# Optimization experiments

Hardware: AMD Instinct MI355X
Metric: run time of the kernel (lower is better)

## Reference

```python
import jax, jax.numpy as jnp
import numpy as np

BATCH, SEQ, D_IN = 4, 2048, 1024
STATE, D_OUT, KX = 1024, 1024, 10


def setup_inputs() -> dict:
    key = jax.random.key(0)
    k0, k1, k2, k3, k4, k5 = jax.random.split(key, 6)
    inputs = jax.random.normal(k0, (BATCH, SEQ, D_IN), jnp.float32)
    h0 = jax.random.normal(k1, (STATE,), jnp.float32)
    A = jax.random.normal(k2, (STATE,), jnp.float32)
    A = A / jnp.max(jnp.abs(A))  # matches init_A / max|init_A|
    B = jax.random.normal(k3, (D_IN, STATE), jnp.float32) / D_IN
    C = jax.random.normal(k4, (STATE, D_OUT), jnp.float32) / STATE
    M = jax.random.normal(k5, (D_IN, D_OUT, KX), jnp.float32) / D_OUT
    return {"inputs": inputs, "h0": h0, "A": A, "B": B, "C": C, "M": M}


def compute_ar_x_preds(w, x):
    # w: (d_out, d_in, k); x: (b, l, d_in)
    d_out, d_in, k = w.shape
    b, l, _ = x.shape
    o = jnp.einsum('oik,bli->bklo', w, x)  # (b, k, l, d_out)
    shifts = jnp.arange(k)
    # roll slice i forward by i along the length axis
    o = jax.vmap(lambda oi, s: jnp.roll(oi, s, axis=1), in_axes=(1, 0), out_axes=1)(o, shifts)
    # triu mask: keep position t in slice i only if t >= i (causal AR)
    m = (jnp.arange(l)[None, :] >= shifts[:, None]).astype(o.dtype)  # (k, l)
    return jnp.sum(o * m[None, :, :, None], axis=1)  # (b, l, d_out)


def reference(inputs, h0, A, B, C, M):
    bsz = inputs.shape[0]
    h_init = jnp.broadcast_to(h0, (bsz, h0.shape[0]))  # h0.expand(bsz, state_dim)
    u_seq = jnp.swapaxes(inputs, 0, 1)  # (l, b, d_in)

    def step(h, u):
        h_new = A * h + u @ B  # diagonal recurrence
        return h_new, h_new

    _, hs = jax.lax.scan(step, h_init, u_seq)  # (l, b, state)
    all_h_t = jnp.swapaxes(hs, 0, 1)  # (b, l, state)
    lds_out = all_h_t @ C  # (b, l, d_out)
    ar = compute_ar_x_preds(M, inputs)
    return lds_out + ar
```

## Files before the change

kernel.cpp:

```cpp
#include <hip/hip_runtime.h>
#include <stdint.h>

typedef unsigned short u16;
typedef __attribute__((ext_vector_type(4))) float f32x4;
typedef __attribute__((ext_vector_type(8))) short s16x8;

#define BATCH 4
#define SEQ   2048
#define DIM   1024
#define KX    10
#define PAD   16
#define SEQP  (SEQ+PAD)

__device__ __forceinline__ u16 f2b(float f) {
    union { float f; uint32_t u; } v; v.f = f;
    uint32_t u = v.u + 0x7fffu + ((v.u >> 16) & 1u);
    return (u16)(u >> 16);
}
__device__ __forceinline__ float b2f(u16 h) {
    union { uint32_t u; float f; } v; v.u = ((uint32_t)h) << 16;
    return v.f;
}

__device__ __forceinline__ void llds16(const u16* g, u16* l) {
    __builtin_amdgcn_global_load_lds(
        (const __attribute__((address_space(1))) uint32_t*)g,
        (__attribute__((address_space(3))) uint32_t*)l, 16, 0, 0);
}

#define PREP_X_END  8256
#define PREP_C_END  10304
#define PREP_M_END  14400

__global__ __launch_bounds__(256) void k_prep(
    const float* __restrict__ x, const float* __restrict__ B,
    const float* __restrict__ C, const float* __restrict__ M,
    u16* __restrict__ Xpad, u16* __restrict__ Btr, u16* __restrict__ Wall)
{
    __shared__ float tile[32][33];
    const int bid = blockIdx.x, tid = threadIdx.x;

    if (bid < PREP_X_END) {
        int idx = bid * 256 + tid;
        long e = (long)idx * 4;
        int i = (int)(e & 1023);
        int row = (int)(e >> 10);
        int t = row % SEQP;
        int b = row / SEQP;
        ushort4 o;
        if (t < PAD) {
            o.x = 0; o.y = 0; o.z = 0; o.w = 0;
        } else {
            const float4 v = *(const float4*)(x + (((long)(b * SEQ + (t - PAD)) << 10) + i));
            o.x = f2b(v.x); o.y = f2b(v.y); o.z = f2b(v.z); o.w = f2b(v.w);
        }
        *(ushort4*)(Xpad + ((long)row << 10) + i) = o;
    } else if (bid < PREP_C_END) {
        const int tb = bid - PREP_X_END;
        const float* in = (tb < 1024) ? B : C;
        u16* out = (tb < 1024) ? Btr : Wall;
        int lb = tb & 1023;
        int bx = lb & 31, by = lb >> 5;
        int tx = tid & 31, ty = tid >> 5;
#pragma unroll
        for (int j = 0; j < 4; j++)
            tile[ty + j * 8][tx] = in[(long)(by * 32 + ty + j * 8) * 1024 + bx * 32 + tx];
        __syncthreads();
#pragma unroll
        for (int j = 0; j < 4; j++)
            out[(long)(bx * 32 + ty + j * 8) * 1024 + by * 32 + tx] = f2b(tile[tx][ty + j * 8]);
    } else {
        int idx = (bid - PREP_C_END) * 256 + tid;
        int o = idx >> 10, i = idx & 1023;
        const float* src = M + (long)idx * KX;
#pragma unroll
        for (int k = 0; k < KX; k++)
            Wall[((long)(k + 1) << 20) + ((long)o << 10) + i] = f2b(src[k]);
    }
}


__global__ void k_scan1(const u16* __restrict__ U, const float* __restrict__ A,
                        float* __restrict__ F) {
    const int sg = threadIdx.x;
    const int bc = blockIdx.x;
    const int b = bc >> 5, c = bc & 31;
    const int s0 = sg << 3;
    const float4 a0 = *(const float4*)(A + s0);
    const float4 a1 = *(const float4*)(A + s0 + 4);
    float a[8] = {a0.x, a0.y, a0.z, a0.w, a1.x, a1.y, a1.z, a1.w};
    float f[8] = {0.f, 0.f, 0.f, 0.f, 0.f, 0.f, 0.f, 0.f};
    const u16* u = U + (((long)(b * SEQ + c * 64)) << 10) + s0;
#pragma unroll 4
    for (int j = 0; j < 64; j++) {
        s16x8 v = *(const s16x8*)(u + ((long)j << 10));
#pragma unroll
        for (int i = 0; i < 8; i++) f[i] = fmaf(a[i], f[i], b2f((u16)v[i]));
    }
    *(float4*)(F + ((long)bc << 10) + s0)     = (float4){f[0], f[1], f[2], f[3]};
    *(float4*)(F + ((long)bc << 10) + s0 + 4) = (float4){f[4], f[5], f[6], f[7]};
}

__global__ void k_scan2(const float* __restrict__ F, const float* __restrict__ A,
                        const float* __restrict__ h0, float* __restrict__ Carry) {
    int idx = blockIdx.x * 256 + threadIdx.x;
    int b = idx >> 10, s = idx & 1023;
    float a = A[s];
    float a64 = a;
#pragma unroll
    for (int q = 0; q < 6; q++) a64 *= a64;
    float carry = h0[s];
#pragma unroll
    for (int c = 0; c < 32; c++) {
        long off = ((long)(b * 32 + c) << 10) + s;
        Carry[off] = carry;
        carry = fmaf(a64, carry, F[off]);
    }
}

__global__ void k_scan3(u16* __restrict__ U, const float* __restrict__ A,
                        const float* __restrict__ Carry) {
    const int sg = threadIdx.x;
    const int bc = blockIdx.x;
    const int b = bc >> 5, c = bc & 31;
    const int s0 = sg << 3;
    const float4 a0 = *(const float4*)(A + s0);
    const float4 a1 = *(const float4*)(A + s0 + 4);
    float a[8] = {a0.x, a0.y, a0.z, a0.w, a1.x, a1.y, a1.z, a1.w};
    float h[8];
#pragma unroll
    for (int i = 0; i < 8; i++) h[i] = Carry[((long)bc << 10) + s0 + i];
    u16* u = U + (((long)(b * SEQ + c * 64)) << 10) + s0;
#pragma unroll 4
    for (int j = 0; j < 64; j++) {
        s16x8 v = *(const s16x8*)(u + ((long)j << 10));
        s16x8 w;
#pragma unroll
        for (int i = 0; i < 8; i++) {
            h[i] = fmaf(a[i], h[i], b2f((u16)v[i]));
            w[i] = (short)f2b(h[i]);
        }
        *(s16x8*)(u + ((long)j << 10)) = w;
    }
}

__global__ __launch_bounds__(256, 4) void k_gemm(
    void* __restrict__ outv, const u16* __restrict__ Xpad,
    const u16* __restrict__ Hbf, const u16* __restrict__ W,
    int ngroups, int use_h, int bf16_out)
{
    __shared__ u16 smem[18432];

    const int tid  = threadIdx.x;
    const int wave = tid >> 6, lane = tid & 63;
    const int pair = wave >> 1, wm = wave & 1;
    const int quad = lane >> 4, l15 = lane & 15;

    const int col0 = blockIdx.x * 64;
    const int row0 = blockIdx.y * 128;
    const int bb = row0 >> 11;
    const long Xrow0 = (long)bb * SEQP + PAD + (row0 & (SEQ - 1));
    const long XslabBase = (Xrow0 - 16) << 10;
    const int lastg = ngroups - 1;

    f32x4 acc[4][4];
#pragma unroll
    for (int i = 0; i < 4; i++)
#pragma unroll
        for (int j = 0; j < 4; j++)
            acc[i][j] = (f32x4){0.f, 0.f, 0.f, 0.f};

    auto stageX2 = [&](int k0) {
#pragma unroll
        for (int p = 0; p < 2; p++) {
            const int kb = k0 + p * 512;
            u16* slab = smem + p * 5120;
#pragma unroll
            for (int q = 0; q < 2; q++) {
                int u = q * 256 + tid;
                int row = u >> 2;
                int kc = (u & 3) ^ ((row >> 1) & 3);
                llds16(Xpad + XslabBase + ((long)row << 10) + kb + kc * 8,
                       &slab[(q * 256 + wave * 64) * 8]);
            }
            {
                int u = 512 + tid;
                int row = u >> 2;
                int kc = (u & 3) ^ ((row >> 1) & 3);
                if (tid < 128)
                    llds16(Xpad + XslabBase + ((long)row << 10) + kb + kc * 8,
                           &slab[(512 + wave * 64) * 8]);
            }
        }
    };
    auto stageW2 = [&](int k0, int wsel, int parity) {
        const u16* Wg = W + ((long)wsel << 20) + ((long)col0 << 10);
#pragma unroll
        for (int p = 0; p < 2; p++) {
            int row = tid >> 2;
            int kc = (tid & 3) ^ ((row >> 1) & 3);
            llds16(Wg + ((long)row << 10) + (k0 + p * 512) + kc * 8,
                   &smem[10240 + (p * 2 + parity) * 2048 + wave * 64 * 8]);
        }
    };
    auto stageH2 = [&](int k0) {
        const u16* Hb = Hbf + ((long)row0 << 10);
#pragma unroll
        for (int p = 0; p < 2; p++) {
            const int kb = k0 + p * 512;
            u16* slab = smem + p * 5120;
#pragma unroll
            for (int q = 0; q < 2; q++) {
                int u = q * 256 + tid;
                int row = u >> 2;
                int kc = (u & 3) ^ ((row >> 1) & 3);
                llds16(Hb + ((long)row << 10) + kb + kc * 8,
                       &slab[(q * 256 + wave * 64) * 8]);
            }
        }
    };

    const u16* slab  = smem + pair * 5120;
    const u16* Wpair = smem + 10240 + pair * 2 * 2048;

    for (int k0 = 0; k0 < 512; k0 += 32) {
        stageX2(k0);
        stageW2(k0, use_h ? 1 : 0, 0);
        __syncthreads();

        for (int g = 0; g < ngroups; g++) {
            const bool isH = use_h && (g == lastg);
            if (isH) {
                stageH2(k0);
                __syncthreads();
            }
            if (g < lastg) {
                int gn = g + 1;
                int wsel = use_h ? ((gn == lastg) ? 0 : gn + 1) : gn;
                stageW2(k0, wsel, gn & 1);
            }

            const int rbase = isH ? 0 : (16 - g);
            const u16* Wrd = Wpair + (g & 1) * 2048;

            s16x8 af[4], bfr[4];
#pragma unroll
            for (int mi = 0; mi < 4; mi++) {
                int arow = rbase + wm * 64 + mi * 16 + l15;
                int kca = (quad ^ ((arow >> 1) & 3)) << 3;
                af[mi] = *(const s16x8*)&slab[arow * 32 + kca];
            }
#pragma unroll
            for (int ni = 0; ni < 4; ni++) {
                int brow = ni * 16 + l15;
                int kcb = (quad ^ ((brow >> 1) & 3)) << 3;
                bfr[ni] = *(const s16x8*)&Wrd[brow * 32 + kcb];
            }
#pragma unroll
            for (int mi = 0; mi < 4; mi++)
#pragma unroll
                for (int ni = 0; ni < 4; ni++)
                    acc[mi][ni] = __builtin_amdgcn_mfma_f32_16x16x32_bf16(
                        af[mi], bfr[ni], acc[mi][ni], 0, 0, 0);
            __syncthreads();
        }
    }

    float* scr = (float*)smem;
    if (pair == 1) {
#pragma unroll
        for (int mi = 0; mi < 4; mi++) {
            int rl = wm * 64 + mi * 16 + quad * 4;
#pragma unroll
            for (int ni = 0; ni < 4; ni++) {
                int c = ni * 16 + l15;
                f32x4 v = acc[mi][ni];
#pragma unroll
                for (int reg = 0; reg < 4; reg++)
                    scr[(rl + reg) * 64 + c] = v[reg];
            }
        }
    }
    __syncthreads();
    if (pair == 0) {
#pragma unroll
        for (int mi = 0; mi < 4; mi++) {
            int rl = wm * 64 + mi * 16 + quad * 4;
            int r = row0 + rl;
#pragma unroll
            for (int ni = 0; ni < 4; ni++) {
                int cl = ni * 16 + l15;
                int c = col0 + cl;
                f32x4 v = acc[mi][ni];
                if (bf16_out) {
                    u16* ob = (u16*)outv;
#pragma unroll
                    for (int reg = 0; reg < 4; reg++)
                        ob[((long)(r + reg) << 10) + c] =
                            f2b(v[reg] + scr[(rl + reg) * 64 + cl]);
                } else {
                    float* of = (float*)outv;
#pragma unroll
                    for (int reg = 0; reg < 4; reg++)
                        of[((long)(r + reg) << 10) + c] =
                            v[reg] + scr[(rl + reg) * 64 + cl];
                }
            }
        }
    }
}


extern "C" void kernel_launch(void* const* d_in, const int* in_sizes, int n_in,
                              void* d_out, int out_size, void* d_ws, size_t ws_size,
                              hipStream_t stream) {
    const float* x  = (const float*)d_in[0];
    const float* h0 = (const float*)d_in[1];
    const float* A  = (const float*)d_in[2];
    const float* B  = (const float*)d_in[3];
    const float* C  = (const float*)d_in[4];
    const float* M  = (const float*)d_in[5];
    float* out = (float*)d_out;

    char* ws = (char*)d_ws;
    u16*   Xpad  = (u16*)  (ws);
    u16*   Wall  = (u16*)  (ws + 16908288);
    u16*   Btr   = (u16*)  (ws + 39976960);
    u16*   Ubf   = (u16*)  (ws + 42074112);
    float* F     = (float*)(ws + 39976960);
    float* Carry = (float*)(ws + 39976960 + 524288);

    k_prep<<<dim3(PREP_M_END), dim3(256), 0, stream>>>(x, B, C, M, Xpad, Btr, Wall);

    k_gemm<<<dim3(16, 64), dim3(256), 0, stream>>>(Ubf, Xpad, Ubf, Btr, 1, 0, 1);

    k_scan1<<<dim3(128), dim3(128), 0, stream>>>(Ubf, A, F);
    k_scan2<<<dim3(16), dim3(256), 0, stream>>>(F, A, h0, Carry);
    k_scan3<<<dim3(128), dim3(128), 0, stream>>>(Ubf, A, Carry);

    k_gemm<<<dim3(16, 64), dim3(256), 0, stream>>>(out, Xpad, Ubf, Wall, 11, 1, 0);
}
```

Baseline: 354.6 us.

## Widen GEMM tile to 128 columns and split scan into finer chunks

The GEMM block tile grows from 128x64 to 128x128, so each wave holds 4x8 accumulators and reuses each A fragment across eight B fragments. This halves redundant X/H staging across column blocks at the cost of more registers, lower occupancy (launch bounds 2) and a two-pass epilogue with a padded scratch stride. Separately, the chunked scan uses 64 chunks of 32 steps instead of 32 of 64, doubling parallelism in the scan1/scan3 passes and lengthening the serial carry pass.

```diff
diff --git a/kernel.cpp b/kernel.cpp
--- a/kernel.cpp
+++ b/kernel.cpp
@@ -84,15 +84,15 @@
                         float* __restrict__ F) {
     const int sg = threadIdx.x;
     const int bc = blockIdx.x;
-    const int b = bc >> 5, c = bc & 31;
+    const int b = bc >> 6, c = bc & 63;
     const int s0 = sg << 3;
     const float4 a0 = *(const float4*)(A + s0);
     const float4 a1 = *(const float4*)(A + s0 + 4);
     float a[8] = {a0.x, a0.y, a0.z, a0.w, a1.x, a1.y, a1.z, a1.w};
     float f[8] = {0.f, 0.f, 0.f, 0.f, 0.f, 0.f, 0.f, 0.f};
-    const u16* u = U + (((long)(b * SEQ + c * 64)) << 10) + s0;
+    const u16* u = U + (((long)(b * SEQ + c * 32)) << 10) + s0;
 #pragma unroll 4
-    for (int j = 0; j < 64; j++) {
+    for (int j = 0; j < 32; j++) {
         s16x8 v = *(const s16x8*)(u + ((long)j << 10));
 #pragma unroll
         for (int i = 0; i < 8; i++) f[i] = fmaf(a[i], f[i], b2f((u16)v[i]));
@@ -106,15 +106,15 @@
     int idx = blockIdx.x * 256 + threadIdx.x;
     int b = idx >> 10, s = idx & 1023;
     float a = A[s];
-    float a64 = a;
-#pragma unroll
-    for (int q = 0; q < 6; q++) a64 *= a64;
+    float a32 = a;
+#pragma unroll
+    for (int q = 0; q < 5; q++) a32 *= a32;
     float carry = h0[s];
 #pragma unroll
-    for (int c = 0; c < 32; c++) {
-        long off = ((long)(b * 32 + c) << 10) + s;
+    for (int c = 0; c < 64; c++) {
+        long off = ((long)(b * 64 + c) << 10) + s;
         Carry[off] = carry;
-        carry = fmaf(a64, carry, F[off]);
+        carry = fmaf(a32, carry, F[off]);
     }
 }
 
@@ -122,7 +122,7 @@
                         const float* __restrict__ Carry) {
     const int sg = threadIdx.x;
     const int bc = blockIdx.x;
-    const int b = bc >> 5, c = bc & 31;
+    const int b = bc >> 6, c = bc & 63;
     const int s0 = sg << 3;
     const float4 a0 = *(const float4*)(A + s0);
     const float4 a1 = *(const float4*)(A + s0 + 4);
@@ -130,9 +130,9 @@
     float h[8];
 #pragma unroll
     for (int i = 0; i < 8; i++) h[i] = Carry[((long)bc << 10) + s0 + i];
-    u16* u = U + (((long)(b * SEQ + c * 64)) << 10) + s0;
+    u16* u = U + (((long)(b * SEQ + c * 32)) << 10) + s0;
 #pragma unroll 4
-    for (int j = 0; j < 64; j++) {
+    for (int j = 0; j < 32; j++) {
         s16x8 v = *(const s16x8*)(u + ((long)j << 10));
         s16x8 w;
 #pragma unroll
@@ -144,30 +144,30 @@
     }
 }
 
-__global__ __launch_bounds__(256, 4) void k_gemm(
+__global__ __launch_bounds__(256, 2) void k_gemm(
     void* __restrict__ outv, const u16* __restrict__ Xpad,
     const u16* __restrict__ Hbf, const u16* __restrict__ W,
     int ngroups, int use_h, int bf16_out)
 {
-    __shared__ u16 smem[18432];
+    __shared__ u16 smem[26624];
 
     const int tid  = threadIdx.x;
     const int wave = tid >> 6, lane = tid & 63;
     const int pair = wave >> 1, wm = wave & 1;
     const int quad = lane >> 4, l15 = lane & 15;
 
-    const int col0 = blockIdx.x * 64;
+    const int col0 = blockIdx.x * 128;
     const int row0 = blockIdx.y * 128;
     const int bb = row0 >> 11;
     const long Xrow0 = (long)bb * SEQP + PAD + (row0 & (SEQ - 1));
     const long XslabBase = (Xrow0 - 16) << 10;
     const int lastg = ngroups - 1;
 
-    f32x4 acc[4][4];
+    f32x4 acc[4][8];
 #pragma unroll
     for (int i = 0; i < 4; i++)
 #pragma unroll
-        for (int j = 0; j < 4; j++)
+        for (int j = 0; j < 8; j++)
             acc[i][j] = (f32x4){0.f, 0.f, 0.f, 0.f};
 
     auto stageX2 = [&](int k0) {
@@ -197,10 +197,14 @@
         const u16* Wg = W + ((long)wsel << 20) + ((long)col0 << 10);
 #pragma unroll
         for (int p = 0; p < 2; p++) {
-            int row = tid >> 2;
-            int kc = (tid & 3) ^ ((row >> 1) & 3);
-            llds16(Wg + ((long)row << 10) + (k0 + p * 512) + kc * 8,
-                   &smem[10240 + (p * 2 + parity) * 2048 + wave * 64 * 8]);
+#pragma unroll
+            for (int q = 0; q < 2; q++) {
+                int u = q * 256 + tid;
+                int row = u >> 2;
+                int kc = (u & 3) ^ ((row >> 1) & 3);
+                llds16(Wg + ((long)row << 10) + (k0 + p * 512) + kc * 8,
+                       &smem[10240 + (p * 2 + parity) * 4096 + (q * 256 + wave * 64) * 8]);
+            }
         }
     };
     auto stageH2 = [&](int k0) {
@@ -221,7 +225,7 @@
     };
 
     const u16* slab  = smem + pair * 5120;
-    const u16* Wpair = smem + 10240 + pair * 2 * 2048;
+    const u16* Wpair = smem + 10240 + pair * 2 * 4096;
 
     for (int k0 = 0; k0 < 512; k0 += 32) {
         stageX2(k0);
@@ -241,72 +245,76 @@
             }
 
             const int rbase = isH ? 0 : (16 - g);
-            const u16* Wrd = Wpair + (g & 1) * 2048;
-
-            s16x8 af[4], bfr[4];
+            const u16* Wrd = Wpair + (g & 1) * 4096;
+
+            s16x8 bfr[8];
+#pragma unroll
+            for (int ni = 0; ni < 8; ni++) {
+                int brow = ni * 16 + l15;
+                int kcb = (quad ^ ((brow >> 1) & 3)) << 3;
+                bfr[ni] = *(const s16x8*)&Wrd[brow * 32 + kcb];
+            }
 #pragma unroll
             for (int mi = 0; mi < 4; mi++) {
                 int arow = rbase + wm * 64 + mi * 16 + l15;
                 int kca = (quad ^ ((arow >> 1) & 3)) << 3;
-                af[mi] = *(const s16x8*)&slab[arow * 32 + kca];
-            }
-#pragma unroll
-            for (int ni = 0; ni < 4; ni++) {
-                int brow = ni * 16 + l15;
-                int kcb = (quad ^ ((brow >> 1) & 3)) << 3;
-                bfr[ni] = *(const s16x8*)&Wrd[brow * 32 + kcb];
-            }
-#pragma unroll
-            for (int mi = 0; mi < 4; mi++)
-#pragma unroll
-                for (int ni = 0; ni < 4; ni++)
+                s16x8 af = *(const s16x8*)&slab[arow * 32 + kca];
+#pragma unroll
+                for (int ni = 0; ni < 8; ni++)
                     acc[mi][ni] = __builtin_amdgcn_mfma_f32_16x16x32_bf16(
-                        af[mi], bfr[ni], acc[mi][ni], 0, 0, 0);
+                        af, bfr[ni], acc[mi][ni], 0, 0, 0);
+            }
             __syncthreads();
         }
     }
 
     float* scr = (float*)smem;
-    if (pair == 1) {
-#pragma unroll
-        for (int mi = 0; mi < 4; mi++) {
-            int rl = wm * 64 + mi * 16 + quad * 4;
-#pragma unroll
-            for (int ni = 0; ni < 4; ni++) {
-                int c = ni * 16 + l15;
-                f32x4 v = acc[mi][ni];
-#pragma unroll
-                for (int reg = 0; reg < 4; reg++)
-                    scr[(rl + reg) * 64 + c] = v[reg];
-            }
-        }
-    }
-    __syncthreads();
-    if (pair == 0) {
-#pragma unroll
-        for (int mi = 0; mi < 4; mi++) {
-            int rl = wm * 64 + mi * 16 + quad * 4;
-            int r = row0 + rl;
-#pragma unroll
-            for (int ni = 0; ni < 4; ni++) {
-                int cl = ni * 16 + l15;
-                int c = col0 + cl;
-                f32x4 v = acc[mi][ni];
-                if (bf16_out) {
-                    u16* ob = (u16*)outv;
+#pragma unroll
+    for (int half = 0; half < 2; half++) {
+        if (pair == 1) {
+#pragma unroll
+            for (int m2 = 0; m2 < 2; m2++) {
+                int mi = half * 2 + m2;
+                int rl = wm * 32 + m2 * 16 + quad * 4;
+#pragma unroll
+                for (int ni = 0; ni < 8; ni++) {
+                    int c = ni * 16 + l15;
+                    f32x4 v = acc[mi][ni];
 #pragma unroll
                     for (int reg = 0; reg < 4; reg++)
-                        ob[((long)(r + reg) << 10) + c] =
-                            f2b(v[reg] + scr[(rl + reg) * 64 + cl]);
-                } else {
-                    float* of = (float*)outv;
-#pragma unroll
-                    for (int reg = 0; reg < 4; reg++)
-                        of[((long)(r + reg) << 10) + c] =
-                            v[reg] + scr[(rl + reg) * 64 + cl];
+                        scr[(rl + reg) * 129 + c] = v[reg];
                 }
             }
         }
+        __syncthreads();
+        if (pair == 0) {
+#pragma unroll
+            for (int m2 = 0; m2 < 2; m2++) {
+                int mi = half * 2 + m2;
+                int rl = wm * 32 + m2 * 16 + quad * 4;
+                int r = row0 + wm * 64 + mi * 16 + quad * 4;
+#pragma unroll
+                for (int ni = 0; ni < 8; ni++) {
+                    int cl = ni * 16 + l15;
+                    int c = col0 + cl;
+                    f32x4 v = acc[mi][ni];
+                    if (bf16_out) {
+                        u16* ob = (u16*)outv;
+#pragma unroll
+                        for (int reg = 0; reg < 4; reg++)
+                            ob[((long)(r + reg) << 10) + c] =
+                                f2b(v[reg] + scr[(rl + reg) * 129 + cl]);
+                    } else {
+                        float* of = (float*)outv;
+#pragma unroll
+                        for (int reg = 0; reg < 4; reg++)
+                            of[((long)(r + reg) << 10) + c] =
+                                v[reg] + scr[(rl + reg) * 129 + cl];
+                    }
+                }
+            }
+        }
+        __syncthreads();
     }
 }
 
@@ -328,15 +336,15 @@
     u16*   Btr   = (u16*)  (ws + 39976960);
     u16*   Ubf   = (u16*)  (ws + 42074112);
     float* F     = (float*)(ws + 39976960);
-    float* Carry = (float*)(ws + 39976960 + 524288);
+    float* Carry = (float*)(ws + 39976960 + 1048576);
 
     k_prep<<<dim3(PREP_M_END), dim3(256), 0, stream>>>(x, B, C, M, Xpad, Btr, Wall);
 
-    k_gemm<<<dim3(16, 64), dim3(256), 0, stream>>>(Ubf, Xpad, Ubf, Btr, 1, 0, 1);
-
-    k_scan1<<<dim3(128), dim3(128), 0, stream>>>(Ubf, A, F);
+    k_gemm<<<dim3(8, 64), dim3(256), 0, stream>>>(Ubf, Xpad, Ubf, Btr, 1, 0, 1);
+
+    k_scan1<<<dim3(256), dim3(128), 0, stream>>>(Ubf, A, F);
     k_scan2<<<dim3(16), dim3(256), 0, stream>>>(F, A, h0, Carry);
-    k_scan3<<<dim3(128), dim3(128), 0, stream>>>(Ubf, A, Carry);
-
-    k_gemm<<<dim3(16, 64), dim3(256), 0, stream>>>(out, Xpad, Ubf, Wall, 11, 1, 0);
-}
+    k_scan3<<<dim3(256), dim3(128), 0, stream>>>(Ubf, A, Carry);
+
+    k_gemm<<<dim3(8, 64), dim3(256), 0, stream>>>(out, Xpad, Ubf, Wall, 11, 1, 0);
+}
```

New measurement: 346.9 us. 2.2% less time.
